# Optimization experiments

Measured on AMD Instinct MI355X. Metric: run time of the kernel, lower is better.

Reference implementation:

```python
import jax, jax.numpy as jnp
import numpy as np

N_NODES = 50000
N_EDGES = 800000
C = 64          # node channels (in_dim == out_dim)
CE = 32         # edge channels
NEG_SLOPE = 0.2


def setup_inputs() -> dict:
    key = jax.random.key(0)
    k1, k2, k3, k4, k5 = jax.random.split(key, 5)
    x = jax.random.normal(k1, (N_NODES, C), dtype=jnp.float32)
    edge_index = jax.random.randint(k2, (2, N_EDGES), 0, N_NODES, dtype=jnp.int64)
    edge_attr = jax.random.normal(k3, (N_EDGES, CE), dtype=jnp.float32)
    # parameters (kaiming-uniform-ish scale)
    wn_bound = float(np.sqrt(6.0 / C))
    weight_node = jax.random.uniform(k4, (C, C), minval=-wn_bound, maxval=wn_bound, dtype=jnp.float32)
    wa_bound = float(np.sqrt(6.0 / (2 * C + CE)))
    weight_triplet_att = jax.random.uniform(k5, (1, 2 * C + CE), minval=-wa_bound, maxval=wa_bound, dtype=jnp.float32)
    bias = jnp.zeros((C,), dtype=jnp.float32)
    return {"x": x, "edge_index": edge_index, "edge_attr": edge_attr,
            "weight_node": weight_node, "weight_triplet_att": weight_triplet_att, "bias": bias}


def reference(x, edge_index, edge_attr, weight_node, weight_triplet_att, bias):
    # x: [N, C], edge_index: [2, E] (row 0 = source j, row 1 = target i), edge_attr: [E, Ce]
    n_nodes = x.shape[0]
    xw = x @ weight_node                      # [N, C]
    src, dst = edge_index[0], edge_index[1]
    x_j = xw[src]                             # [E, C] messages from source
    x_i = xw[dst]                             # [E, C] target features
    triplet = jnp.concatenate([x_i, edge_attr, x_j], axis=-1)   # [E, 2C+Ce]
    alpha = (triplet * weight_triplet_att).sum(axis=-1)          # [E]
    alpha = jax.nn.leaky_relu(alpha, NEG_SLOPE)
    # segment softmax over edges grouped by destination node (PyG softmax)
    seg_max = jax.ops.segment_max(alpha, dst, num_segments=n_nodes)  # [N]
    alpha = jnp.exp(alpha - seg_max[dst])
    seg_sum = jax.ops.segment_sum(alpha, dst, num_segments=n_nodes)  # [N]
    alpha = alpha / (seg_sum[dst] + 1e-16)
    msg = alpha[:, None] * x_j                                      # [E, C]
    out = jax.ops.segment_sum(msg, dst, num_segments=n_nodes)       # [N, C]
    return out + bias
```

## Files before the change

kernel.cpp:

```cpp
#include <hip/hip_runtime.h>
#include <math.h>

#define N_NODES 50000
#define N_EDGES 800000
#define C 64
#define CE 32
#define NEG_SLOPE 0.2f

#define SLOT 64
#define SLOT_SHIFT 6

#define BN 256
#define BN_SHIFT 8
#define NB ((N_NODES + BN - 1) / BN)
#define TILE 1024
#define EPT (TILE / 256)
#define CAP 5120
#define GC_STRIDE 16

#define K1_BLOCKS 1024
#define NROWG ((N_NODES + 3) / 4)

__device__ __forceinline__ unsigned bf16_rne(float f) {
    unsigned u = __float_as_uint(f);
    return (u + 0x7FFFu + ((u >> 16) & 1u)) >> 16;
}

__global__ __launch_bounds__(256) void k1_xw(
    const float* __restrict__ x, const float* __restrict__ W,
    const float* __restrict__ watt,
    unsigned short* __restrict__ xwb, float* __restrict__ a_i, float* __restrict__ a_j,
    unsigned* __restrict__ gcur)
{
    int lane = threadIdx.x & 63;
    int warp = threadIdx.x >> 6;
    if (blockIdx.x == 0)
        for (int i = threadIdx.x; i < NB * GC_STRIDE; i += 256) gcur[i] = 0u;
    float Wc[64];
#pragma unroll
    for (int k = 0; k < 64; k++) Wc[k] = W[k * 64 + lane];
    float wi = watt[lane], wj = watt[96 + lane];
    for (int rg = blockIdx.x; rg < NROWG; rg += gridDim.x) {
        int row = rg * 4 + warp;
        if (row >= N_NODES) continue;
        int row_u = __builtin_amdgcn_readfirstlane(row);
        const float* xr = x + (size_t)row_u * C;
        float a0 = 0.f, a1 = 0.f, a2 = 0.f, a3 = 0.f;
#pragma unroll
        for (int k = 0; k < 64; k += 4) {
            float s0 = xr[k], s1 = xr[k + 1], s2 = xr[k + 2], s3 = xr[k + 3];
            a0 = fmaf(s0, Wc[k],     a0);
            a1 = fmaf(s1, Wc[k + 1], a1);
            a2 = fmaf(s2, Wc[k + 2], a2);
            a3 = fmaf(s3, Wc[k + 3], a3);
        }
        float acc = (a0 + a1) + (a2 + a3);
        xwb[(size_t)row * C + lane] = (unsigned short)bf16_rne(acc);
        float vi = acc * wi;
        float vj = acc * wj;
#pragma unroll
        for (int off = 32; off; off >>= 1) {
            vi += __shfl_down(vi, off, 64);
            vj += __shfl_down(vj, off, 64);
        }
        if (lane == 0) { a_i[row] = vi; a_j[row] = vj; }
    }
}

__global__ __launch_bounds__(256) void k2_bin(
    const int* __restrict__ eidx, const float* __restrict__ edge_attr,
    const float* __restrict__ watt, const float* __restrict__ a_j,
    unsigned* __restrict__ gcur, uint2* __restrict__ bbuf)
{
    __shared__ unsigned hcnt[NB], gslot[NB];
    int tid = threadIdx.x;
    size_t tb = (size_t)blockIdx.x * TILE;
    for (int i = tid; i < NB; i += 256) hcnt[i] = 0u;
    __syncthreads();

    float av[EPT]; unsigned key[EPT];
#pragma unroll
    for (int k = 0; k < EPT; k++) {
        size_t e = tb + (size_t)k * 256 + tid;
        bool ok = e < (size_t)N_EDGES;
        size_t ee = ok ? e : 0;
        int src = eidx[ee];
        int dst = eidx[N_EDGES + ee];
        const float4* ea = (const float4*)(edge_attr + ee * CE);
        float ec = 0.f;
#pragma unroll
        for (int q = 0; q < CE / 4; q++) {
            float4 v = ea[q];
            ec += v.x * watt[64 + 4 * q + 0] + v.y * watt[64 + 4 * q + 1] +
                  v.z * watt[64 + 4 * q + 2] + v.w * watt[64 + 4 * q + 3];
        }
        av[k] = ec + a_j[src];
        key[k] = ok ? (((unsigned)src << 16) | (unsigned)dst) : 0xFFFFFFFFu;
        if (ok) atomicAdd(&hcnt[(unsigned)dst >> BN_SHIFT], 1u);
    }
    __syncthreads();

    for (int b = tid; b < NB; b += 256) {
        unsigned h = hcnt[b];
        gslot[b] = h ? atomicAdd(&gcur[b * GC_STRIDE], h) : 0u;
    }
    __syncthreads();

#pragma unroll
    for (int k = 0; k < EPT; k++) {
        if (key[k] != 0xFFFFFFFFu) {
            unsigned b = (key[k] & 0xFFFFu) >> BN_SHIFT;
            unsigned slot = atomicAdd(&gslot[b], 1u);
            if (slot < (unsigned)CAP)
                bbuf[(size_t)b * CAP + slot] = make_uint2(__float_as_uint(av[k]), key[k]);
        }
    }
}

__global__ __launch_bounds__(256) void k3_rank(
    const unsigned* __restrict__ gcur, const uint2* __restrict__ bbuf,
    const float* __restrict__ a_i,
    unsigned* __restrict__ count, float* __restrict__ den,
    unsigned* __restrict__ sorted)
{
    __shared__ unsigned lcnt[BN];
    __shared__ float lden[BN];
    int b = blockIdx.x, tid = threadIdx.x;
    lcnt[tid] = 0u; lden[tid] = 0.f;
    __syncthreads();
    unsigned tot = gcur[b * GC_STRIDE];
    tot = tot > (unsigned)CAP ? (unsigned)CAP : tot;
    const uint2* seg = bbuf + (size_t)b * CAP;
    for (unsigned i = tid; i < tot; i += 256) {
        uint2 v = seg[i];
        unsigned dst = v.y & 0xFFFFu;
        unsigned src = v.y >> 16;
        float al = a_i[dst] + __uint_as_float(v.x);
        al = al > 0.f ? al : NEG_SLOPE * al;
        float w = __expf(al);
        unsigned ln = dst & (BN - 1);
        unsigned r = atomicAdd(&lcnt[ln], 1u);
        if (r < (unsigned)SLOT) {
            sorted[((size_t)dst << SLOT_SHIFT) + r] = (src << 16) | bf16_rne(w);
            atomicAdd(&lden[ln], w);
        }
    }
    __syncthreads();
    unsigned node = ((unsigned)b << BN_SHIFT) + tid;
    if (node < N_NODES) {
        unsigned c = lcnt[tid];
        count[node] = c > (unsigned)SLOT ? (unsigned)SLOT : c;
        den[node] = lden[tid];
    }
}

__global__ __launch_bounds__(256) void k5_gather(
    const unsigned* __restrict__ count, const float* __restrict__ den,
    const unsigned* __restrict__ sorted,
    const unsigned short* __restrict__ xwb, const float* __restrict__ bias,
    float* __restrict__ out)
{
    int warp = threadIdx.x >> 6, lane = threadIdx.x & 63;
    int node = blockIdx.x * 4 + warp;
    if (node >= N_NODES) return;
    int group = lane >> 3, sub = lane & 7;
    unsigned c = count[node];
    unsigned pk = 0u;
    if (lane < (int)c) pk = sorted[((unsigned)node << SLOT_SHIFT) + lane];
    float acc[8];
#pragma unroll
    for (int i = 0; i < 8; i++) acc[i] = 0.f;
    unsigned iters = (c + 7) >> 3;
    for (unsigned it = 0; it < iters; it++) {
        int t = (int)(it * 8) + group;
        unsigned p = (unsigned)__shfl((int)pk, t, 64);
        float w = __uint_as_float(p << 16);
        unsigned s = p >> 16;
        uint4 v = ((const uint4*)(xwb + (size_t)s * C))[sub];
        acc[0] += w * __uint_as_float(v.x << 16);
        acc[1] += w * __uint_as_float(v.x & 0xFFFF0000u);
        acc[2] += w * __uint_as_float(v.y << 16);
        acc[3] += w * __uint_as_float(v.y & 0xFFFF0000u);
        acc[4] += w * __uint_as_float(v.z << 16);
        acc[5] += w * __uint_as_float(v.z & 0xFFFF0000u);
        acc[6] += w * __uint_as_float(v.w << 16);
        acc[7] += w * __uint_as_float(v.w & 0xFFFF0000u);
    }
#pragma unroll
    for (int off = 8; off < 64; off <<= 1) {
#pragma unroll
        for (int i = 0; i < 8; i++) acc[i] += __shfl_xor(acc[i], off, 64);
    }
    float rden = 1.0f / (den[node] + 1e-16f);
    if (group == 0) {
        float4 b4a = ((const float4*)bias)[sub * 2];
        float4 b4b = ((const float4*)bias)[sub * 2 + 1];
        float4 o1, o2;
        o1.x = acc[0] * rden + b4a.x; o1.y = acc[1] * rden + b4a.y;
        o1.z = acc[2] * rden + b4a.z; o1.w = acc[3] * rden + b4a.w;
        o2.x = acc[4] * rden + b4b.x; o2.y = acc[5] * rden + b4b.y;
        o2.z = acc[6] * rden + b4b.z; o2.w = acc[7] * rden + b4b.w;
        ((float4*)(out + (size_t)node * C))[sub * 2] = o1;
        ((float4*)(out + (size_t)node * C))[sub * 2 + 1] = o2;
    }
}

extern "C" void kernel_launch(void* const* d_in, const int* in_sizes, int n_in,
                              void* d_out, int out_size, void* d_ws, size_t ws_size,
                              hipStream_t stream) {
    const float* x         = (const float*)d_in[0];
    const int*   eidx      = (const int*)d_in[1];
    const float* edge_attr = (const float*)d_in[2];
    const float* W         = (const float*)d_in[3];
    const float* watt      = (const float*)d_in[4];
    const float* bias      = (const float*)d_in[5];
    float* out = (float*)d_out;

    char* ws = (char*)d_ws;
    size_t off = 0;
    auto alloc = [&](size_t bytes) -> void* {
        void* p = ws + off;
        off += (bytes + 255) & ~(size_t)255;
        return p;
    };
    unsigned short* xwb  = (unsigned short*)alloc((size_t)N_NODES * C * 2);
    float*    a_i    = (float*)alloc(N_NODES * 4);
    float*    a_j    = (float*)alloc(N_NODES * 4);
    unsigned* gcur   = (unsigned*)alloc((size_t)NB * GC_STRIDE * 4);
    uint2*    bbuf   = (uint2*)alloc((size_t)NB * CAP * 8);
    unsigned* count  = (unsigned*)alloc(N_NODES * 4);
    float*    den    = (float*)alloc(N_NODES * 4);
    unsigned* sorted = (unsigned*)alloc((size_t)N_NODES * SLOT * 4);

    k1_xw<<<K1_BLOCKS, 256, 0, stream>>>(x, W, watt, xwb, a_i, a_j, gcur);
    k2_bin<<<(N_EDGES + TILE - 1) / TILE, 256, 0, stream>>>(eidx, edge_attr, watt,
                                                            a_j, gcur, bbuf);
    k3_rank<<<NB, 256, 0, stream>>>(gcur, bbuf, a_i, count, den, sorted);
    k5_gather<<<(N_NODES + 3) / 4, 256, 0, stream>>>(count, den, sorted, xwb, bias, out);
}
```

Baseline: 251.0 us.

## Replace global atomic bucket cursors with per-tile fixed-capacity bucket cells

The binning pass no longer uses global atomics to reserve space in destination buckets. Each edge tile (now 4096 edges) writes into its own fixed-capacity cell per bucket and records a per-tile count, and the rank kernel walks all tile cells for its 128-node bucket. This removes the contended global atomics and the gcur zeroing. In exchange the rank kernel has to scan about 196 small cells per bucket. Any cell holding more than 40 edges silently drops the extra edges; the expected load is about 10.5 per cell, so overflow is unlikely but possible.

```diff
diff --git a/kernel.cpp b/kernel.cpp
--- a/kernel.cpp
+++ b/kernel.cpp
@@ -10,13 +10,12 @@
 #define SLOT 64
 #define SLOT_SHIFT 6
 
-#define BN 256
-#define BN_SHIFT 8
-#define NB ((N_NODES + BN - 1) / BN)
-#define TILE 1024
-#define EPT (TILE / 256)
-#define CAP 5120
-#define GC_STRIDE 16
+#define NB 391
+#define BN_SHIFT 7
+
+#define TILE 4096
+#define NT ((N_EDGES + TILE - 1) / TILE)
+#define CAPC 40
 
 #define K1_BLOCKS 1024
 #define NROWG ((N_NODES + 3) / 4)
@@ -29,13 +28,10 @@
 __global__ __launch_bounds__(256) void k1_xw(
     const float* __restrict__ x, const float* __restrict__ W,
     const float* __restrict__ watt,
-    unsigned short* __restrict__ xwb, float* __restrict__ a_i, float* __restrict__ a_j,
-    unsigned* __restrict__ gcur)
+    unsigned short* __restrict__ xwb, float* __restrict__ a_i, float* __restrict__ a_j)
 {
     int lane = threadIdx.x & 63;
     int warp = threadIdx.x >> 6;
-    if (blockIdx.x == 0)
-        for (int i = threadIdx.x; i < NB * GC_STRIDE; i += 256) gcur[i] = 0u;
     float Wc[64];
 #pragma unroll
     for (int k = 0; k < 64; k++) Wc[k] = W[k * 64 + lane];
@@ -70,87 +66,81 @@
 __global__ __launch_bounds__(256) void k2_bin(
     const int* __restrict__ eidx, const float* __restrict__ edge_attr,
     const float* __restrict__ watt, const float* __restrict__ a_j,
-    unsigned* __restrict__ gcur, uint2* __restrict__ bbuf)
-{
-    __shared__ unsigned hcnt[NB], gslot[NB];
+    uint2* __restrict__ bbuf, unsigned* __restrict__ tcnt)
+{
+    __shared__ unsigned lcur[NB];
     int tid = threadIdx.x;
-    size_t tb = (size_t)blockIdx.x * TILE;
-    for (int i = tid; i < NB; i += 256) hcnt[i] = 0u;
-    __syncthreads();
-
-    float av[EPT]; unsigned key[EPT];
-#pragma unroll
-    for (int k = 0; k < EPT; k++) {
+    int t = blockIdx.x;
+    for (int b = tid; b < NB; b += 256) lcur[b] = 0u;
+    __syncthreads();
+    size_t tb = (size_t)t * TILE;
+#pragma unroll 2
+    for (int k = 0; k < TILE / 256; k++) {
         size_t e = tb + (size_t)k * 256 + tid;
-        bool ok = e < (size_t)N_EDGES;
-        size_t ee = ok ? e : 0;
-        int src = eidx[ee];
-        int dst = eidx[N_EDGES + ee];
-        const float4* ea = (const float4*)(edge_attr + ee * CE);
-        float ec = 0.f;
-#pragma unroll
-        for (int q = 0; q < CE / 4; q++) {
-            float4 v = ea[q];
-            ec += v.x * watt[64 + 4 * q + 0] + v.y * watt[64 + 4 * q + 1] +
-                  v.z * watt[64 + 4 * q + 2] + v.w * watt[64 + 4 * q + 3];
-        }
-        av[k] = ec + a_j[src];
-        key[k] = ok ? (((unsigned)src << 16) | (unsigned)dst) : 0xFFFFFFFFu;
-        if (ok) atomicAdd(&hcnt[(unsigned)dst >> BN_SHIFT], 1u);
-    }
-    __syncthreads();
-
+        if (e < (size_t)N_EDGES) {
+            int src = eidx[e];
+            int dst = eidx[N_EDGES + e];
+            const float4* ea = (const float4*)(edge_attr + e * CE);
+            float ec = 0.f;
+#pragma unroll
+            for (int q = 0; q < CE / 4; q++) {
+                float4 v = ea[q];
+                ec += v.x * watt[64 + 4 * q + 0] + v.y * watt[64 + 4 * q + 1] +
+                      v.z * watt[64 + 4 * q + 2] + v.w * watt[64 + 4 * q + 3];
+            }
+            float av = ec + a_j[src];
+            unsigned b = (unsigned)dst >> BN_SHIFT;
+            unsigned slot = atomicAdd(&lcur[b], 1u);
+            if (slot < (unsigned)CAPC)
+                bbuf[((size_t)b * NT + t) * CAPC + slot] =
+                    make_uint2(__float_as_uint(av), ((unsigned)src << 16) | (unsigned)dst);
+        }
+    }
+    __syncthreads();
     for (int b = tid; b < NB; b += 256) {
-        unsigned h = hcnt[b];
-        gslot[b] = h ? atomicAdd(&gcur[b * GC_STRIDE], h) : 0u;
-    }
-    __syncthreads();
-
-#pragma unroll
-    for (int k = 0; k < EPT; k++) {
-        if (key[k] != 0xFFFFFFFFu) {
-            unsigned b = (key[k] & 0xFFFFu) >> BN_SHIFT;
-            unsigned slot = atomicAdd(&gslot[b], 1u);
-            if (slot < (unsigned)CAP)
-                bbuf[(size_t)b * CAP + slot] = make_uint2(__float_as_uint(av[k]), key[k]);
-        }
+        unsigned c = lcur[b];
+        tcnt[(size_t)t * NB + b] = c > (unsigned)CAPC ? (unsigned)CAPC : c;
     }
 }
 
 __global__ __launch_bounds__(256) void k3_rank(
-    const unsigned* __restrict__ gcur, const uint2* __restrict__ bbuf,
+    const uint2* __restrict__ bbuf, const unsigned* __restrict__ tcnt,
     const float* __restrict__ a_i,
     unsigned* __restrict__ count, float* __restrict__ den,
     unsigned* __restrict__ sorted)
 {
-    __shared__ unsigned lcnt[BN];
-    __shared__ float lden[BN];
+    __shared__ unsigned lcnt[128];
+    __shared__ float lden[128];
     int b = blockIdx.x, tid = threadIdx.x;
-    lcnt[tid] = 0u; lden[tid] = 0.f;
-    __syncthreads();
-    unsigned tot = gcur[b * GC_STRIDE];
-    tot = tot > (unsigned)CAP ? (unsigned)CAP : tot;
-    const uint2* seg = bbuf + (size_t)b * CAP;
-    for (unsigned i = tid; i < tot; i += 256) {
-        uint2 v = seg[i];
-        unsigned dst = v.y & 0xFFFFu;
-        unsigned src = v.y >> 16;
-        float al = a_i[dst] + __uint_as_float(v.x);
-        al = al > 0.f ? al : NEG_SLOPE * al;
-        float w = __expf(al);
-        unsigned ln = dst & (BN - 1);
-        unsigned r = atomicAdd(&lcnt[ln], 1u);
-        if (r < (unsigned)SLOT) {
-            sorted[((size_t)dst << SLOT_SHIFT) + r] = (src << 16) | bf16_rne(w);
-            atomicAdd(&lden[ln], w);
-        }
-    }
-    __syncthreads();
-    unsigned node = ((unsigned)b << BN_SHIFT) + tid;
-    if (node < N_NODES) {
-        unsigned c = lcnt[tid];
-        count[node] = c > (unsigned)SLOT ? (unsigned)SLOT : c;
-        den[node] = lden[tid];
+    if (tid < 128) { lcnt[tid] = 0u; lden[tid] = 0.f; }
+    __syncthreads();
+    int warp = tid >> 6, lane = tid & 63;
+    for (int t = warp; t < NT; t += 4) {
+        unsigned cnt = tcnt[(size_t)t * NB + b];
+        const uint2* cell = bbuf + ((size_t)b * NT + t) * CAPC;
+        for (unsigned i = lane; i < cnt; i += 64) {
+            uint2 v = cell[i];
+            unsigned dst = v.y & 0xFFFFu;
+            unsigned src = v.y >> 16;
+            float al = a_i[dst] + __uint_as_float(v.x);
+            al = al > 0.f ? al : NEG_SLOPE * al;
+            float w = __expf(al);
+            unsigned ln = dst & 127u;
+            unsigned r = atomicAdd(&lcnt[ln], 1u);
+            if (r < (unsigned)SLOT) {
+                sorted[((size_t)dst << SLOT_SHIFT) + r] = (src << 16) | bf16_rne(w);
+                atomicAdd(&lden[ln], w);
+            }
+        }
+    }
+    __syncthreads();
+    if (tid < 128) {
+        unsigned node = ((unsigned)b << BN_SHIFT) + (unsigned)tid;
+        if (node < N_NODES) {
+            unsigned c = lcnt[tid];
+            count[node] = c > (unsigned)SLOT ? (unsigned)SLOT : c;
+            den[node] = lden[tid];
+        }
     }
 }
 
@@ -223,18 +213,17 @@
         off += (bytes + 255) & ~(size_t)255;
         return p;
     };
-    unsigned short* xwb  = (unsigned short*)alloc((size_t)N_NODES * C * 2);
+    unsigned short* xwb = (unsigned short*)alloc((size_t)N_NODES * C * 2);
     float*    a_i    = (float*)alloc(N_NODES * 4);
     float*    a_j    = (float*)alloc(N_NODES * 4);
-    unsigned* gcur   = (unsigned*)alloc((size_t)NB * GC_STRIDE * 4);
-    uint2*    bbuf   = (uint2*)alloc((size_t)NB * CAP * 8);
+    uint2*    bbuf   = (uint2*)alloc((size_t)NB * NT * CAPC * 8);
+    unsigned* tcnt   = (unsigned*)alloc((size_t)NT * NB * 4);
     unsigned* count  = (unsigned*)alloc(N_NODES * 4);
     float*    den    = (float*)alloc(N_NODES * 4);
     unsigned* sorted = (unsigned*)alloc((size_t)N_NODES * SLOT * 4);
 
-    k1_xw<<<K1_BLOCKS, 256, 0, stream>>>(x, W, watt, xwb, a_i, a_j, gcur);
-    k2_bin<<<(N_EDGES + TILE - 1) / TILE, 256, 0, stream>>>(eidx, edge_attr, watt,
-                                                            a_j, gcur, bbuf);
-    k3_rank<<<NB, 256, 0, stream>>>(gcur, bbuf, a_i, count, den, sorted);
+    k1_xw<<<K1_BLOCKS, 256, 0, stream>>>(x, W, watt, xwb, a_i, a_j);
+    k2_bin<<<NT, 256, 0, stream>>>(eidx, edge_attr, watt, a_j, bbuf, tcnt);
+    k3_rank<<<NB, 256, 0, stream>>>(bbuf, tcnt, a_i, count, den, sorted);
     k5_gather<<<(N_NODES + 3) / 4, 256, 0, stream>>>(count, den, sorted, xwb, bias, out);
 }
```

Result: slower. 300.9 us (+19.9%).

## Shard bin counters across replicas and compute softmax denominator in gather

Applied to the files above, without the earlier changes.

Splits each destination bucket's global cursor into 8 replicas, chosen by tile index, so fewer blocks contend on the same global atomic in the binning kernel. Each replica has its own smaller capacity region. The rank kernel loops over the replicas. The per-node denominator is no longer built with shared-memory float atomics and stored; the gather kernel instead sums the bf16-rounded weights with a wave reduction. This removes the den array and its LDS atomics, but it uses rounded weights and adds overflow risk if a replica exceeds its capacity.

```diff
diff --git a/kernel.cpp b/kernel.cpp
--- a/kernel.cpp
+++ b/kernel.cpp
@@ -13,9 +13,13 @@
 #define BN 256
 #define BN_SHIFT 8
 #define NB ((N_NODES + BN - 1) / BN)
+
 #define TILE 1024
 #define EPT (TILE / 256)
-#define CAP 5120
+#define NT ((N_EDGES + TILE - 1) / TILE)
+
+#define NR 8
+#define CAPR 768
 #define GC_STRIDE 16
 
 #define K1_BLOCKS 1024
@@ -32,10 +36,12 @@
     unsigned short* __restrict__ xwb, float* __restrict__ a_i, float* __restrict__ a_j,
     unsigned* __restrict__ gcur)
 {
+    for (size_t i = (size_t)blockIdx.x * 256 + threadIdx.x;
+         i < (size_t)NB * NR * GC_STRIDE; i += (size_t)K1_BLOCKS * 256)
+        gcur[i] = 0u;
+
     int lane = threadIdx.x & 63;
     int warp = threadIdx.x >> 6;
-    if (blockIdx.x == 0)
-        for (int i = threadIdx.x; i < NB * GC_STRIDE; i += 256) gcur[i] = 0u;
     float Wc[64];
 #pragma unroll
     for (int k = 0; k < 64; k++) Wc[k] = W[k * 64 + lane];
@@ -72,12 +78,14 @@
     const float* __restrict__ watt, const float* __restrict__ a_j,
     unsigned* __restrict__ gcur, uint2* __restrict__ bbuf)
 {
-    __shared__ unsigned hcnt[NB], gslot[NB];
+    __shared__ unsigned hcnt[NB], gb[NB], lcur[NB];
     int tid = threadIdx.x;
-    size_t tb = (size_t)blockIdx.x * TILE;
-    for (int i = tid; i < NB; i += 256) hcnt[i] = 0u;
-    __syncthreads();
-
+    int t = blockIdx.x;
+    int r = t & (NR - 1);
+    for (int b = tid; b < NB; b += 256) { hcnt[b] = 0u; lcur[b] = 0u; }
+    __syncthreads();
+
+    size_t tb = (size_t)t * TILE;
     float av[EPT]; unsigned key[EPT];
 #pragma unroll
     for (int k = 0; k < EPT; k++) {
@@ -102,7 +110,7 @@
 
     for (int b = tid; b < NB; b += 256) {
         unsigned h = hcnt[b];
-        gslot[b] = h ? atomicAdd(&gcur[b * GC_STRIDE], h) : 0u;
+        gb[b] = h ? atomicAdd(&gcur[(b * NR + r) * GC_STRIDE], h) : 0u;
     }
     __syncthreads();
 
@@ -110,9 +118,10 @@
     for (int k = 0; k < EPT; k++) {
         if (key[k] != 0xFFFFFFFFu) {
             unsigned b = (key[k] & 0xFFFFu) >> BN_SHIFT;
-            unsigned slot = atomicAdd(&gslot[b], 1u);
-            if (slot < (unsigned)CAP)
-                bbuf[(size_t)b * CAP + slot] = make_uint2(__float_as_uint(av[k]), key[k]);
+            unsigned slot = gb[b] + atomicAdd(&lcur[b], 1u);
+            if (slot < (unsigned)CAPR)
+                bbuf[((size_t)(b * NR + r)) * CAPR + slot] =
+                    make_uint2(__float_as_uint(av[k]), key[k]);
         }
     }
 }
@@ -120,43 +129,38 @@
 __global__ __launch_bounds__(256) void k3_rank(
     const unsigned* __restrict__ gcur, const uint2* __restrict__ bbuf,
     const float* __restrict__ a_i,
-    unsigned* __restrict__ count, float* __restrict__ den,
-    unsigned* __restrict__ sorted)
+    unsigned* __restrict__ count, unsigned* __restrict__ sorted)
 {
     __shared__ unsigned lcnt[BN];
-    __shared__ float lden[BN];
     int b = blockIdx.x, tid = threadIdx.x;
-    lcnt[tid] = 0u; lden[tid] = 0.f;
-    __syncthreads();
-    unsigned tot = gcur[b * GC_STRIDE];
-    tot = tot > (unsigned)CAP ? (unsigned)CAP : tot;
-    const uint2* seg = bbuf + (size_t)b * CAP;
-    for (unsigned i = tid; i < tot; i += 256) {
-        uint2 v = seg[i];
-        unsigned dst = v.y & 0xFFFFu;
-        unsigned src = v.y >> 16;
-        float al = a_i[dst] + __uint_as_float(v.x);
-        al = al > 0.f ? al : NEG_SLOPE * al;
-        float w = __expf(al);
-        unsigned ln = dst & (BN - 1);
-        unsigned r = atomicAdd(&lcnt[ln], 1u);
-        if (r < (unsigned)SLOT) {
-            sorted[((size_t)dst << SLOT_SHIFT) + r] = (src << 16) | bf16_rne(w);
-            atomicAdd(&lden[ln], w);
-        }
-    }
-    __syncthreads();
-    unsigned node = ((unsigned)b << BN_SHIFT) + tid;
+    lcnt[tid] = 0u;
+    __syncthreads();
+    for (int r = 0; r < NR; r++) {
+        unsigned cnt = gcur[(b * NR + r) * GC_STRIDE];
+        cnt = cnt > (unsigned)CAPR ? (unsigned)CAPR : cnt;
+        const uint2* seg = bbuf + ((size_t)(b * NR + r)) * CAPR;
+        for (unsigned i = tid; i < cnt; i += 256) {
+            uint2 v = seg[i];
+            unsigned dst = v.y & 0xFFFFu;
+            unsigned src = v.y >> 16;
+            float al = a_i[dst] + __uint_as_float(v.x);
+            al = al > 0.f ? al : NEG_SLOPE * al;
+            float w = __expf(al);
+            unsigned rk = atomicAdd(&lcnt[dst & (BN - 1)], 1u);
+            if (rk < (unsigned)SLOT)
+                sorted[((size_t)dst << SLOT_SHIFT) + rk] = (src << 16) | bf16_rne(w);
+        }
+    }
+    __syncthreads();
+    unsigned node = ((unsigned)b << BN_SHIFT) + (unsigned)tid;
     if (node < N_NODES) {
         unsigned c = lcnt[tid];
         count[node] = c > (unsigned)SLOT ? (unsigned)SLOT : c;
-        den[node] = lden[tid];
     }
 }
 
 __global__ __launch_bounds__(256) void k5_gather(
-    const unsigned* __restrict__ count, const float* __restrict__ den,
-    const unsigned* __restrict__ sorted,
+    const unsigned* __restrict__ count, const unsigned* __restrict__ sorted,
     const unsigned short* __restrict__ xwb, const float* __restrict__ bias,
     float* __restrict__ out)
 {
@@ -167,6 +171,7 @@
     unsigned c = count[node];
     unsigned pk = 0u;
     if (lane < (int)c) pk = sorted[((unsigned)node << SLOT_SHIFT) + lane];
+    float wpart = __uint_as_float(pk << 16);
     float acc[8];
 #pragma unroll
     for (int i = 0; i < 8; i++) acc[i] = 0.f;
@@ -191,7 +196,10 @@
 #pragma unroll
         for (int i = 0; i < 8; i++) acc[i] += __shfl_xor(acc[i], off, 64);
     }
-    float rden = 1.0f / (den[node] + 1e-16f);
+#pragma unroll
+    for (int off = 1; off < 64; off <<= 1)
+        wpart += __shfl_xor(wpart, off, 64);
+    float rden = 1.0f / (wpart + 1e-16f);
     if (group == 0) {
         float4 b4a = ((const float4*)bias)[sub * 2];
         float4 b4b = ((const float4*)bias)[sub * 2 + 1];
@@ -223,18 +231,16 @@
         off += (bytes + 255) & ~(size_t)255;
         return p;
     };
-    unsigned short* xwb  = (unsigned short*)alloc((size_t)N_NODES * C * 2);
+    unsigned short* xwb = (unsigned short*)alloc((size_t)N_NODES * C * 2);
     float*    a_i    = (float*)alloc(N_NODES * 4);
     float*    a_j    = (float*)alloc(N_NODES * 4);
-    unsigned* gcur   = (unsigned*)alloc((size_t)NB * GC_STRIDE * 4);
-    uint2*    bbuf   = (uint2*)alloc((size_t)NB * CAP * 8);
+    unsigned* gcur   = (unsigned*)alloc((size_t)NB * NR * GC_STRIDE * 4);
+    uint2*    bbuf   = (uint2*)alloc((size_t)NB * NR * CAPR * 8);
     unsigned* count  = (unsigned*)alloc(N_NODES * 4);
-    float*    den    = (float*)alloc(N_NODES * 4);
     unsigned* sorted = (unsigned*)alloc((size_t)N_NODES * SLOT * 4);
 
     k1_xw<<<K1_BLOCKS, 256, 0, stream>>>(x, W, watt, xwb, a_i, a_j, gcur);
-    k2_bin<<<(N_EDGES + TILE - 1) / TILE, 256, 0, stream>>>(eidx, edge_attr, watt,
-                                                            a_j, gcur, bbuf);
-    k3_rank<<<NB, 256, 0, stream>>>(gcur, bbuf, a_i, count, den, sorted);
-    k5_gather<<<(N_NODES + 3) / 4, 256, 0, stream>>>(count, den, sorted, xwb, bias, out);
-}
+    k2_bin<<<NT, 256, 0, stream>>>(eidx, edge_attr, watt, a_j, gcur, bbuf);
+    k3_rank<<<NB, BN, 0, stream>>>(gcur, bbuf, a_i, count, sorted);
+    k5_gather<<<(N_NODES + 3) / 4, 256, 0, stream>>>(count, sorted, xwb, bias, out);
+}
```

Measured after the change: 255.4 us. Within noise of the previous version (+1.8%).
